# Performance work log

Hardware: AMD Instinct MI355X
Metric: run time of the kernel (lower is better)

Reference implementation:

```python
import jax, jax.numpy as jnp
import numpy as np

HEADS = 8
DIM_HEAD = 32
SCALE = DIM_HEAD ** -0.5


def setup_inputs() -> dict:
    key = jax.random.key(0)
    ks = jax.random.split(key, 5)
    b, c, H, W = 4, 256, 48, 48
    n = H * W
    hidden = HEADS * DIM_HEAD
    x = jax.random.normal(ks[0], (b, c, H, W), dtype=jnp.float32)
    pos_bias = jax.random.normal(ks[1], (HEADS, n, n), dtype=jnp.float32) * 0.02
    w_qkv = jax.random.normal(ks[2], (hidden * 3, c), dtype=jnp.float32) * (c ** -0.5)
    w_out = jax.random.normal(ks[3], (c, hidden), dtype=jnp.float32) * (hidden ** -0.5)
    b_out = jax.random.normal(ks[4], (c,), dtype=jnp.float32) * 0.01
    return {"x": x, "pos_bias": pos_bias, "w_qkv": w_qkv, "w_out": w_out, "b_out": b_out}


def reference(x, pos_bias, w_qkv, w_out, b_out):
    b, c, H, W = x.shape
    n = H * W
    xf = x.reshape(b, c, n)                                  # [b, c, n]
    qkv = jnp.einsum('oc,bcn->bon', w_qkv, xf)               # 1x1 conv, no bias
    q, k, v = jnp.split(qkv, 3, axis=1)                      # each [b, hidden, n]
    def to_heads(t):
        return t.reshape(b, HEADS, DIM_HEAD, n)              # b h d n
    q, k, v = to_heads(q) * SCALE, to_heads(k), to_heads(v)
    sim = jnp.einsum('bhdi,bhdj->bhij', q, k)                # [b, h, n, n]
    sim = sim + pos_bias[None]                               # broadcast over batch
    attn = jax.nn.softmax(sim, axis=-1)
    out = jnp.einsum('bhij,bhdj->bhid', attn, v)             # [b, h, n, d]
    out = out.transpose(0, 1, 3, 2).reshape(b, HEADS * DIM_HEAD, n)  # b (h d) n
    out = jnp.einsum('oc,bcn->bon', w_out, out) + b_out[None, :, None]
    return out.reshape(b, c, H, W)
```

## Files before the change

### kernel.cpp

```cpp
#include <hip/hip_runtime.h>
#include <stdint.h>
#include <stddef.h>

#define BB 4
#define CC 256
#define NH 8
#define DH 32
#define NN 2304
#define O3 768
#define HID 256
#define QK_SCALE 0.17677669529663687f
#define LOG2E 1.44269504f

typedef __attribute__((ext_vector_type(8))) short short8;
typedef __attribute__((ext_vector_type(4))) float float4v;

__device__ __forceinline__ unsigned short f2bf(float f) {
    union { float f; uint32_t u; } v; v.f = f;
    uint32_t u = v.u;
    return (unsigned short)((u + 0x7FFFu + ((u >> 16) & 1u)) >> 16);
}
__device__ __forceinline__ float bf2f(unsigned short s) {
    union { uint32_t u; float f; } v; v.u = ((uint32_t)s) << 16;
    return v.f;
}

__global__ __launch_bounds__(256) void prep_kernel(const float* __restrict__ x,
                                                   const float* __restrict__ wqkv,
                                                   const float* __restrict__ wout,
                                                   unsigned short* __restrict__ xT,
                                                   unsigned short* __restrict__ whi,
                                                   unsigned short* __restrict__ wlo,
                                                   unsigned short* __restrict__ wob) {
    const int bid = blockIdx.x;
    const int t = threadIdx.x;
    if (bid < 2304) {
        const int n0 = (bid % 72) * 32, c0 = ((bid / 72) % 8) * 32, b = bid / 576;
        __shared__ float ls[32][33];
        {
            int c = t >> 3, nc = (t & 7) * 4;
            float4 v4 = *(const float4*)(x + ((size_t)b * CC + c0 + c) * NN + n0 + nc);
            ls[c][nc] = v4.x; ls[c][nc + 1] = v4.y; ls[c][nc + 2] = v4.z; ls[c][nc + 3] = v4.w;
        }
        __syncthreads();
        {
            int n = t >> 3, cl = (t & 7) * 4;
            uint32_t p0 = (uint32_t)f2bf(ls[cl + 0][n]) | ((uint32_t)f2bf(ls[cl + 1][n]) << 16);
            uint32_t p1 = (uint32_t)f2bf(ls[cl + 2][n]) | ((uint32_t)f2bf(ls[cl + 3][n]) << 16);
            uint32_t* dst = (uint32_t*)(xT + ((size_t)b * NN + n0 + n) * CC + c0 + cl);
            dst[0] = p0; dst[1] = p1;
        }
    } else {
        int i = (bid - 2304) * 256 + t;
        float wv = wqkv[i];
        unsigned short hi = f2bf(wv);
        whi[i] = hi;
        wlo[i] = f2bf(wv - bf2f(hi));
        if (i < HID * HID) wob[i] = f2bf(wout[i]);
    }
}

__global__ __launch_bounds__(256) void qkv_gemm_bf16(const unsigned short* __restrict__ xT,
                                                     const unsigned short* __restrict__ whi,
                                                     const unsigned short* __restrict__ wlo,
                                                     unsigned short* __restrict__ q,
                                                     unsigned short* __restrict__ k,
                                                     unsigned short* __restrict__ v) {
    const int og = blockIdx.x;
    const int n0 = blockIdx.y * 64;
    const int b  = blockIdx.z;
    const int t = threadIdx.x;
    const int w = t >> 6, lane = t & 63, l15 = lane & 15, quad = lane >> 4;
    const unsigned short* xb = xT + (size_t)b * NN * CC;

    float4v acc[4] = {{0.f,0.f,0.f,0.f},{0.f,0.f,0.f,0.f},
                      {0.f,0.f,0.f,0.f},{0.f,0.f,0.f,0.f}};

    if (og < 8) {
        const int o0 = og * 64;
        const unsigned short* ap = xb + (size_t)(n0 + w * 16 + l15) * CC + quad * 8;
        #pragma unroll
        for (int c0 = 0; c0 < CC; c0 += 32) {
            short8 af = *(const short8*)(ap + c0);
            #pragma unroll
            for (int jj = 0; jj < 4; ++jj) {
                const size_t wo = (size_t)(o0 + jj * 16 + l15) * CC + c0 + quad * 8;
                short8 bh = *(const short8*)(whi + wo);
                short8 bl = *(const short8*)(wlo + wo);
                acc[jj] = __builtin_amdgcn_mfma_f32_16x16x32_bf16(af, bh, acc[jj], 0, 0, 0);
                acc[jj] = __builtin_amdgcn_mfma_f32_16x16x32_bf16(af, bl, acc[jj], 0, 0, 0);
            }
        }
        #pragma unroll
        for (int jj = 0; jj < 4; ++jj) {
            const int o = o0 + jj * 16 + l15;
            const int which = o >> 8;
            const int h = (o >> 5) & 7, d = o & 31;
            unsigned short* dst = which ? k : q;
            const float sc = which ? 1.0f : QK_SCALE * LOG2E;
            #pragma unroll
            for (int r = 0; r < 4; ++r) {
                const int n = n0 + w * 16 + quad * 4 + r;
                dst[(((size_t)b * NH + h) * NN + n) * DH + d] = f2bf(acc[jj][r] * sc);
            }
        }
    } else {
        const int o0 = 512 + (og - 8) * 64;
        const size_t wr = (size_t)(o0 + w * 16 + l15) * CC + quad * 8;
        #pragma unroll
        for (int c0 = 0; c0 < CC; c0 += 32) {
            short8 ah = *(const short8*)(whi + wr + c0);
            short8 al = *(const short8*)(wlo + wr + c0);
            #pragma unroll
            for (int jj = 0; jj < 4; ++jj) {
                short8 bf = *(const short8*)(xb + (size_t)(n0 + jj * 16 + l15) * CC + c0 + quad * 8);
                acc[jj] = __builtin_amdgcn_mfma_f32_16x16x32_bf16(ah, bf, acc[jj], 0, 0, 0);
                acc[jj] = __builtin_amdgcn_mfma_f32_16x16x32_bf16(al, bf, acc[jj], 0, 0, 0);
            }
        }
        #pragma unroll
        for (int r = 0; r < 4; ++r) {
            const int o = o0 + w * 16 + quad * 4 + r;
            const int h = (o >> 5) & 7, d = o & 31;
            #pragma unroll
            for (int jj = 0; jj < 4; ++jj) {
                const int n = n0 + jj * 16 + l15;
                v[(((size_t)b * NH + h) * DH + d) * NN + n] = f2bf(acc[jj][r]);
            }
        }
    }
}

__global__ __launch_bounds__(256) void attn_kernel(const unsigned short* __restrict__ qg,
                                                   const unsigned short* __restrict__ kg,
                                                   const unsigned short* __restrict__ vg,
                                                   const float* __restrict__ bias,
                                                   unsigned short* __restrict__ ao) {
    const int i0   = blockIdx.x * 16;
    const int h    = blockIdx.y;
    const int t    = threadIdx.x;
    const int b    = t >> 6;
    const int lane = t & 63;
    const int l15  = lane & 15;
    const int quad = lane >> 4;

    __shared__ __align__(16) unsigned short bls[2][16][132];
    __shared__ __align__(16) unsigned short ps[BB][16][136];

    const size_t bh = (size_t)b * NH + h;
    const unsigned short* qp = qg + bh * NN * DH;
    const unsigned short* kp = kg + bh * NN * DH;
    const unsigned short* vp = vg + bh * DH * NN;

    short8 qf = *(const short8*)(qp + (size_t)(i0 + l15) * DH + quad * 8);

    float4v oa0 = {0.f, 0.f, 0.f, 0.f};
    float4v oa1 = {0.f, 0.f, 0.f, 0.f};
    float4v zero = {0.f, 0.f, 0.f, 0.f};
    float l_r[4] = {0.f, 0.f, 0.f, 0.f};

    const float* bsrc = bias + ((size_t)h * NN + i0) * NN;
    const int srow = t >> 5;
    const int scol = (t & 31) * 4;

    {
        float4 a = *(const float4*)(bsrc + (size_t)srow * NN + scol);
        float4 c = *(const float4*)(bsrc + (size_t)(srow + 8) * NN + scol);
        uint32_t* d0 = (uint32_t*)&bls[0][srow][scol];
        d0[0] = (uint32_t)f2bf(a.x * LOG2E) | ((uint32_t)f2bf(a.y * LOG2E) << 16);
        d0[1] = (uint32_t)f2bf(a.z * LOG2E) | ((uint32_t)f2bf(a.w * LOG2E) << 16);
        uint32_t* d1 = (uint32_t*)&bls[0][srow + 8][scol];
        d1[0] = (uint32_t)f2bf(c.x * LOG2E) | ((uint32_t)f2bf(c.y * LOG2E) << 16);
        d1[1] = (uint32_t)f2bf(c.z * LOG2E) | ((uint32_t)f2bf(c.w * LOG2E) << 16);
    }
    __syncthreads();

    int cur = 0;
    for (int jt = 0; jt < NN; jt += 128) {
        const int jtn = jt + 128;
        const bool have = (jtn < NN);
        float4 a, c;
        if (have) {
            a = *(const float4*)(bsrc + (size_t)srow * NN + jtn + scol);
            c = *(const float4*)(bsrc + (size_t)(srow + 8) * NN + jtn + scol);
        }

        float bc[4][8];
        #pragma unroll
        for (int r = 0; r < 4; ++r)
            #pragma unroll
            for (int jj = 0; jj < 8; ++jj)
                bc[r][jj] = bf2f(bls[cur][quad * 4 + r][jj * 16 + l15]);

        float4v s[8];
        #pragma unroll
        for (int jj = 0; jj < 8; ++jj) {
            short8 kf = *(const short8*)(kp + (size_t)(jt + jj * 16 + l15) * DH + quad * 8);
            s[jj] = __builtin_amdgcn_mfma_f32_16x16x32_bf16(qf, kf, zero, 0, 0, 0);
        }

        #pragma unroll
        for (int r = 0; r < 4; ++r) {
            const int row = quad * 4 + r;
            #pragma unroll
            for (int jj = 0; jj < 8; ++jj) {
                float p = exp2f(s[jj][r] + bc[r][jj]);
                l_r[r] += p;
                ps[b][row][jj * 16 + l15] = f2bf(p);
            }
        }

        #pragma unroll
        for (int cc = 0; cc < 4; ++cc) {
            short8 pa = *(const short8*)&ps[b][l15][cc * 32 + quad * 8];
            short8 v0 = *(const short8*)(vp + (size_t)l15 * NN        + jt + cc * 32 + quad * 8);
            short8 v1 = *(const short8*)(vp + (size_t)(l15 + 16) * NN + jt + cc * 32 + quad * 8);
            oa0 = __builtin_amdgcn_mfma_f32_16x16x32_bf16(pa, v0, oa0, 0, 0, 0);
            oa1 = __builtin_amdgcn_mfma_f32_16x16x32_bf16(pa, v1, oa1, 0, 0, 0);
        }

        if (have) {
            const int nxt = cur ^ 1;
            uint32_t* d0 = (uint32_t*)&bls[nxt][srow][scol];
            d0[0] = (uint32_t)f2bf(a.x * LOG2E) | ((uint32_t)f2bf(a.y * LOG2E) << 16);
            d0[1] = (uint32_t)f2bf(a.z * LOG2E) | ((uint32_t)f2bf(a.w * LOG2E) << 16);
            uint32_t* d1 = (uint32_t*)&bls[nxt][srow + 8][scol];
            d1[0] = (uint32_t)f2bf(c.x * LOG2E) | ((uint32_t)f2bf(c.y * LOG2E) << 16);
            d1[1] = (uint32_t)f2bf(c.z * LOG2E) | ((uint32_t)f2bf(c.w * LOG2E) << 16);
        }
        __syncthreads();
        cur ^= 1;
    }

    #pragma unroll
    for (int r = 0; r < 4; ++r) {
        #pragma unroll
        for (int off = 1; off < 16; off <<= 1)
            l_r[r] += __shfl_xor(l_r[r], off, 64);
    }

    unsigned short* aop = ao + ((size_t)b * NN + i0) * HID + h * DH;
    #pragma unroll
    for (int r = 0; r < 4; ++r) {
        const int row = quad * 4 + r;
        const float inv = 1.0f / l_r[r];
        aop[(size_t)row * HID + l15]      = f2bf(oa0[r] * inv);
        aop[(size_t)row * HID + 16 + l15] = f2bf(oa1[r] * inv);
    }
}

__global__ __launch_bounds__(256) void out_proj(const unsigned short* __restrict__ wob,
                                                const unsigned short* __restrict__ aob,
                                                const float* __restrict__ bout,
                                                float* __restrict__ out) {
    const int n0 = blockIdx.x * 64;
    const int o0 = blockIdx.y * 64;
    const int b  = blockIdx.z;
    const int t = threadIdx.x;
    const int w = t >> 6, lane = t & 63, l15 = lane & 15, quad = lane >> 4;
    const int orow = o0 + w * 16;

    float4v acc[4] = {{0.f,0.f,0.f,0.f},{0.f,0.f,0.f,0.f},
                      {0.f,0.f,0.f,0.f},{0.f,0.f,0.f,0.f}};
    const unsigned short* ap = aob + ((size_t)b * NN + n0) * HID;
    #pragma unroll
    for (int c0 = 0; c0 < HID; c0 += 32) {
        short8 af = *(const short8*)(wob + (size_t)(orow + l15) * HID + c0 + quad * 8);
        #pragma unroll
        for (int jj = 0; jj < 4; ++jj) {
            short8 bf = *(const short8*)(ap + (size_t)(jj * 16 + l15) * HID + c0 + quad * 8);
            acc[jj] = __builtin_amdgcn_mfma_f32_16x16x32_bf16(af, bf, acc[jj], 0, 0, 0);
        }
    }
    float* op = out + (size_t)b * HID * NN;
    #pragma unroll
    for (int r = 0; r < 4; ++r) {
        const int o = orow + quad * 4 + r;
        const float bv = bout[o];
        #pragma unroll
        for (int jj = 0; jj < 4; ++jj)
            op[(size_t)o * NN + n0 + jj * 16 + l15] = acc[jj][r] + bv;
    }
}

extern "C" void kernel_launch(void* const* d_in, const int* in_sizes, int n_in,
                              void* d_out, int out_size, void* d_ws, size_t ws_size,
                              hipStream_t stream) {
    const float* x        = (const float*)d_in[0];
    const float* pos_bias = (const float*)d_in[1];
    const float* w_qkv    = (const float*)d_in[2];
    const float* w_out    = (const float*)d_in[3];
    const float* b_out    = (const float*)d_in[4];
    float* out = (float*)d_out;

    char* ws = (char*)d_ws;
    unsigned short* q   = (unsigned short*)(ws);
    unsigned short* k   = (unsigned short*)(ws + 4718592);
    unsigned short* v   = (unsigned short*)(ws + 9437184);
    unsigned short* ao  = (unsigned short*)(ws + 14155776);
    unsigned short* wob = (unsigned short*)(ws + 18874368);
    unsigned short* whi = (unsigned short*)(ws + 19005440);
    unsigned short* wlo = (unsigned short*)(ws + 19398656);
    unsigned short* xT  = (unsigned short*)(ws + 19791872);

    prep_kernel<<<3072, 256, 0, stream>>>(x, w_qkv, w_out, xT, whi, wlo, wob);
    qkv_gemm_bf16<<<dim3(12, NN / 64, BB), 256, 0, stream>>>(xT, whi, wlo, q, k, v);
    attn_kernel<<<dim3(NN / 16, NH), 256, 0, stream>>>(q, k, v, pos_bias, ao);
    out_proj<<<dim3(NN / 64, HID / 64, BB), 256, 0, stream>>>(wob, ao, b_out, out);
}
```

Before: 431.2 us.

## Process 32 query rows per attention block and fold bias into MFMA accumulator

The attention kernel now handles two 16-row query sub-tiles per block, so each loaded K and V fragment is reused twice and the number of blocks streaming K/V is halved. The bias tile is stored in LDS in the MFMA accumulator layout and passed as the C input of the QK MFMA, which removes the separate add. K and V loads are hoisted to the top of each iteration, and probabilities are packed to bf16 with v_cvt_pk_bf16_f32. The costs are more registers per thread (launch bounds now target 3 blocks per CU) and half as many blocks in the grid.

```diff
diff --git a/kernel.cpp b/kernel.cpp
--- a/kernel.cpp
+++ b/kernel.cpp
@@ -22,6 +22,10 @@
 }
 __device__ __forceinline__ float bf2f(unsigned short s) {
     union { uint32_t u; float f; } v; v.u = ((uint32_t)s) << 16;
+    return v.f;
+}
+__device__ __forceinline__ float bits2f(uint32_t u) {
+    union { uint32_t u; float f; } v; v.u = u;
     return v.f;
 }
 
@@ -131,12 +135,12 @@
     }
 }
 
-__global__ __launch_bounds__(256) void attn_kernel(const unsigned short* __restrict__ qg,
-                                                   const unsigned short* __restrict__ kg,
-                                                   const unsigned short* __restrict__ vg,
-                                                   const float* __restrict__ bias,
-                                                   unsigned short* __restrict__ ao) {
-    const int i0   = blockIdx.x * 16;
+__global__ __launch_bounds__(256, 3) void attn_kernel(const unsigned short* __restrict__ qg,
+                                                      const unsigned short* __restrict__ kg,
+                                                      const unsigned short* __restrict__ vg,
+                                                      const float* __restrict__ bias,
+                                                      unsigned short* __restrict__ ao) {
+    const int i0   = blockIdx.x * 32;
     const int h    = blockIdx.y;
     const int t    = threadIdx.x;
     const int b    = t >> 6;
@@ -144,108 +148,147 @@
     const int l15  = lane & 15;
     const int quad = lane >> 4;
 
-    __shared__ __align__(16) unsigned short bls[2][16][132];
-    __shared__ __align__(16) unsigned short ps[BB][16][136];
+    __shared__ unsigned short bias_l[2][2][64][34];
+    __shared__ unsigned short ps[BB][16][136];
 
     const size_t bh = (size_t)b * NH + h;
     const unsigned short* qp = qg + bh * NN * DH;
     const unsigned short* kp = kg + bh * NN * DH;
     const unsigned short* vp = vg + bh * DH * NN;
 
-    short8 qf = *(const short8*)(qp + (size_t)(i0 + l15) * DH + quad * 8);
-
-    float4v oa0 = {0.f, 0.f, 0.f, 0.f};
-    float4v oa1 = {0.f, 0.f, 0.f, 0.f};
-    float4v zero = {0.f, 0.f, 0.f, 0.f};
-    float l_r[4] = {0.f, 0.f, 0.f, 0.f};
-
-    const float* bsrc = bias + ((size_t)h * NN + i0) * NN;
-    const int srow = t >> 5;
-    const int scol = (t & 31) * 4;
-
-    {
-        float4 a = *(const float4*)(bsrc + (size_t)srow * NN + scol);
-        float4 c = *(const float4*)(bsrc + (size_t)(srow + 8) * NN + scol);
-        uint32_t* d0 = (uint32_t*)&bls[0][srow][scol];
-        d0[0] = (uint32_t)f2bf(a.x * LOG2E) | ((uint32_t)f2bf(a.y * LOG2E) << 16);
-        d0[1] = (uint32_t)f2bf(a.z * LOG2E) | ((uint32_t)f2bf(a.w * LOG2E) << 16);
-        uint32_t* d1 = (uint32_t*)&bls[0][srow + 8][scol];
-        d1[0] = (uint32_t)f2bf(c.x * LOG2E) | ((uint32_t)f2bf(c.y * LOG2E) << 16);
-        d1[1] = (uint32_t)f2bf(c.z * LOG2E) | ((uint32_t)f2bf(c.w * LOG2E) << 16);
-    }
+    short8 qf0 = *(const short8*)(qp + (size_t)(i0 + l15) * DH + quad * 8);
+    short8 qf1 = *(const short8*)(qp + (size_t)(i0 + 16 + l15) * DH + quad * 8);
+
+    float4v oa00 = {0.f,0.f,0.f,0.f}, oa01 = {0.f,0.f,0.f,0.f};
+    float4v oa10 = {0.f,0.f,0.f,0.f}, oa11 = {0.f,0.f,0.f,0.f};
+    float l_r[2][4] = {{0.f,0.f,0.f,0.f},{0.f,0.f,0.f,0.f}};
+
+    const int a2    = t >> 4;
+    const int scol  = (t & 15) * 8;
+    const int sub_s = a2 >> 3;
+    const int ln_b  = ((a2 & 7) >> 1) * 16 + (scol & 15);
+    const int e_b   = 4 * (scol >> 4) + 2 * (a2 & 1);
+    const float* brow0 = bias + ((size_t)h * NN + i0 + 2 * a2) * NN;
+    const float* brow1 = brow0 + NN;
+
+#define BIAS_STAGE(BUF, JT)                                                        \
+{                                                                                  \
+    float4 x0 = *(const float4*)(brow0 + (JT) + scol);                             \
+    float4 x1 = *(const float4*)(brow0 + (JT) + scol + 4);                         \
+    float4 y0 = *(const float4*)(brow1 + (JT) + scol);                             \
+    float4 y1 = *(const float4*)(brow1 + (JT) + scol + 4);                         \
+    _Pragma("unroll")                                                              \
+    for (int i = 0; i < 4; ++i) {                                                  \
+        float xe0 = ((const float*)&x0)[i] * LOG2E, ye0 = ((const float*)&y0)[i] * LOG2E; \
+        float xe1 = ((const float*)&x1)[i] * LOG2E, ye1 = ((const float*)&y1)[i] * LOG2E; \
+        uint32_t p0 = (uint32_t)f2bf(xe0) | ((uint32_t)f2bf(ye0) << 16);           \
+        uint32_t p1 = (uint32_t)f2bf(xe1) | ((uint32_t)f2bf(ye1) << 16);           \
+        *(uint32_t*)&bias_l[BUF][sub_s][ln_b + i][e_b]     = p0;                   \
+        *(uint32_t*)&bias_l[BUF][sub_s][ln_b + 4 + i][e_b] = p1;                   \
+    }                                                                              \
+}
+
+    BIAS_STAGE(0, 0)
     __syncthreads();
 
     int cur = 0;
     for (int jt = 0; jt < NN; jt += 128) {
         const int jtn = jt + 128;
         const bool have = (jtn < NN);
-        float4 a, c;
+
+        short8 vv[8];
+        #pragma unroll
+        for (int cc = 0; cc < 4; ++cc) {
+            vv[2*cc]   = *(const short8*)(vp + (size_t)l15 * NN        + jt + cc*32 + quad*8);
+            vv[2*cc+1] = *(const short8*)(vp + (size_t)(l15+16) * NN   + jt + cc*32 + quad*8);
+        }
+        short8 kf[8];
+        #pragma unroll
+        for (int jj = 0; jj < 8; ++jj)
+            kf[jj] = *(const short8*)(kp + (size_t)(jt + jj*16 + l15) * DH + quad*8);
+        float4 nx0, nx1, ny0, ny1;
         if (have) {
-            a = *(const float4*)(bsrc + (size_t)srow * NN + jtn + scol);
-            c = *(const float4*)(bsrc + (size_t)(srow + 8) * NN + jtn + scol);
-        }
-
-        float bc[4][8];
-        #pragma unroll
-        for (int r = 0; r < 4; ++r)
-            #pragma unroll
-            for (int jj = 0; jj < 8; ++jj)
-                bc[r][jj] = bf2f(bls[cur][quad * 4 + r][jj * 16 + l15]);
-
-        float4v s[8];
-        #pragma unroll
-        for (int jj = 0; jj < 8; ++jj) {
-            short8 kf = *(const short8*)(kp + (size_t)(jt + jj * 16 + l15) * DH + quad * 8);
-            s[jj] = __builtin_amdgcn_mfma_f32_16x16x32_bf16(qf, kf, zero, 0, 0, 0);
-        }
-
-        #pragma unroll
-        for (int r = 0; r < 4; ++r) {
-            const int row = quad * 4 + r;
+            nx0 = *(const float4*)(brow0 + jtn + scol);
+            nx1 = *(const float4*)(brow0 + jtn + scol + 4);
+            ny0 = *(const float4*)(brow1 + jtn + scol);
+            ny1 = *(const float4*)(brow1 + jtn + scol + 4);
+        }
+
+        #pragma unroll
+        for (int sub = 0; sub < 2; ++sub) {
+            const short8 qf = sub ? qf1 : qf0;
+            float4v s[8];
             #pragma unroll
             for (int jj = 0; jj < 8; ++jj) {
-                float p = exp2f(s[jj][r] + bc[r][jj]);
-                l_r[r] += p;
-                ps[b][row][jj * 16 + l15] = f2bf(p);
-            }
-        }
-
-        #pragma unroll
-        for (int cc = 0; cc < 4; ++cc) {
-            short8 pa = *(const short8*)&ps[b][l15][cc * 32 + quad * 8];
-            short8 v0 = *(const short8*)(vp + (size_t)l15 * NN        + jt + cc * 32 + quad * 8);
-            short8 v1 = *(const short8*)(vp + (size_t)(l15 + 16) * NN + jt + cc * 32 + quad * 8);
-            oa0 = __builtin_amdgcn_mfma_f32_16x16x32_bf16(pa, v0, oa0, 0, 0, 0);
-            oa1 = __builtin_amdgcn_mfma_f32_16x16x32_bf16(pa, v1, oa1, 0, 0, 0);
+                uint32_t u0 = *(const uint32_t*)&bias_l[cur][sub][lane][4*jj];
+                uint32_t u1 = *(const uint32_t*)&bias_l[cur][sub][lane][4*jj + 2];
+                float4v ci = { bits2f(u0 << 16), bits2f(u0 & 0xffff0000u),
+                               bits2f(u1 << 16), bits2f(u1 & 0xffff0000u) };
+                s[jj] = __builtin_amdgcn_mfma_f32_16x16x32_bf16(qf, kf[jj], ci, 0, 0, 0);
+            }
+            #pragma unroll
+            for (int r = 0; r < 4; ++r) {
+                const int row = quad * 4 + r;
+                float pv_[8];
+                #pragma unroll
+                for (int jj = 0; jj < 8; ++jj) { pv_[jj] = exp2f(s[jj][r]); l_r[sub][r] += pv_[jj]; }
+                #pragma unroll
+                for (int jp = 0; jp < 4; ++jp) {
+                    uint32_t pk;
+                    asm("v_cvt_pk_bf16_f32 %0, %1, %2" : "=v"(pk) : "v"(pv_[2*jp]), "v"(pv_[2*jp+1]));
+                    ps[b][row][(2*jp)   * 16 + l15] = (unsigned short)pk;
+                    ps[b][row][(2*jp+1) * 16 + l15] = (unsigned short)(pk >> 16);
+                }
+            }
+            #pragma unroll
+            for (int cc = 0; cc < 4; ++cc) {
+                short8 pa = *(const short8*)&ps[b][l15][cc * 32 + quad * 8];
+                if (sub == 0) {
+                    oa00 = __builtin_amdgcn_mfma_f32_16x16x32_bf16(pa, vv[2*cc],   oa00, 0, 0, 0);
+                    oa01 = __builtin_amdgcn_mfma_f32_16x16x32_bf16(pa, vv[2*cc+1], oa01, 0, 0, 0);
+                } else {
+                    oa10 = __builtin_amdgcn_mfma_f32_16x16x32_bf16(pa, vv[2*cc],   oa10, 0, 0, 0);
+                    oa11 = __builtin_amdgcn_mfma_f32_16x16x32_bf16(pa, vv[2*cc+1], oa11, 0, 0, 0);
+                }
+            }
         }
 
         if (have) {
             const int nxt = cur ^ 1;
-            uint32_t* d0 = (uint32_t*)&bls[nxt][srow][scol];
-            d0[0] = (uint32_t)f2bf(a.x * LOG2E) | ((uint32_t)f2bf(a.y * LOG2E) << 16);
-            d0[1] = (uint32_t)f2bf(a.z * LOG2E) | ((uint32_t)f2bf(a.w * LOG2E) << 16);
-            uint32_t* d1 = (uint32_t*)&bls[nxt][srow + 8][scol];
-            d1[0] = (uint32_t)f2bf(c.x * LOG2E) | ((uint32_t)f2bf(c.y * LOG2E) << 16);
-            d1[1] = (uint32_t)f2bf(c.z * LOG2E) | ((uint32_t)f2bf(c.w * LOG2E) << 16);
+            #pragma unroll
+            for (int i = 0; i < 4; ++i) {
+                float xe0 = ((const float*)&nx0)[i] * LOG2E, ye0 = ((const float*)&ny0)[i] * LOG2E;
+                float xe1 = ((const float*)&nx1)[i] * LOG2E, ye1 = ((const float*)&ny1)[i] * LOG2E;
+                uint32_t p0 = (uint32_t)f2bf(xe0) | ((uint32_t)f2bf(ye0) << 16);
+                uint32_t p1 = (uint32_t)f2bf(xe1) | ((uint32_t)f2bf(ye1) << 16);
+                *(uint32_t*)&bias_l[nxt][sub_s][ln_b + i][e_b]     = p0;
+                *(uint32_t*)&bias_l[nxt][sub_s][ln_b + 4 + i][e_b] = p1;
+            }
         }
         __syncthreads();
         cur ^= 1;
     }
+#undef BIAS_STAGE
 
     #pragma unroll
-    for (int r = 0; r < 4; ++r) {
-        #pragma unroll
-        for (int off = 1; off < 16; off <<= 1)
-            l_r[r] += __shfl_xor(l_r[r], off, 64);
-    }
+    for (int sub = 0; sub < 2; ++sub)
+        #pragma unroll
+        for (int r = 0; r < 4; ++r) {
+            #pragma unroll
+            for (int off = 1; off < 16; off <<= 1)
+                l_r[sub][r] += __shfl_xor(l_r[sub][r], off, 64);
+        }
 
     unsigned short* aop = ao + ((size_t)b * NN + i0) * HID + h * DH;
     #pragma unroll
     for (int r = 0; r < 4; ++r) {
-        const int row = quad * 4 + r;
-        const float inv = 1.0f / l_r[r];
-        aop[(size_t)row * HID + l15]      = f2bf(oa0[r] * inv);
-        aop[(size_t)row * HID + 16 + l15] = f2bf(oa1[r] * inv);
+        const int row0 = quad * 4 + r;
+        const float inv0 = 1.0f / l_r[0][r];
+        const float inv1 = 1.0f / l_r[1][r];
+        aop[(size_t)row0 * HID + l15]             = f2bf(oa00[r] * inv0);
+        aop[(size_t)row0 * HID + 16 + l15]        = f2bf(oa01[r] * inv0);
+        aop[(size_t)(row0 + 16) * HID + l15]      = f2bf(oa10[r] * inv1);
+        aop[(size_t)(row0 + 16) * HID + 16 + l15] = f2bf(oa11[r] * inv1);
     }
 }
 
@@ -305,6 +348,6 @@
 
     prep_kernel<<<3072, 256, 0, stream>>>(x, w_qkv, w_out, xT, whi, wlo, wob);
     qkv_gemm_bf16<<<dim3(12, NN / 64, BB), 256, 0, stream>>>(xT, whi, wlo, q, k, v);
-    attn_kernel<<<dim3(NN / 16, NH), 256, 0, stream>>>(q, k, v, pos_bias, ao);
+    attn_kernel<<<dim3(NN / 32, NH), 256, 0, stream>>>(q, k, v, pos_bias, ao);
     out_proj<<<dim3(NN / 64, HID / 64, BB), 256, 0, stream>>>(wob, ao, b_out, out);
 }
```

Result: slower. 493.3 us (+14.4%).
